# Optimization experiments

Hardware: AMD Instinct MI355X
Metric: run time of the kernel (lower is better)

## Reference

```python
import jax, jax.numpy as jnp
import numpy as np

T = 0.09   # softmax temperature
M = 0.7    # momentum for key-encoder update
DIM, K, B, L, P = 128, 65536, 1024, 512, 8388608

def _l2norm(x, axis):
    return x / jnp.linalg.norm(x, axis=axis, keepdims=True)

def setup_inputs() -> dict:
    key = jax.random.key(0)
    ks = jax.random.split(key, 6)
    q = jax.random.normal(ks[0], (B, DIM), jnp.float32)
    queue = _l2norm(jax.random.normal(ks[1], (DIM, K), jnp.float32), axis=0)  # columns normalized as in __init__
    keys = jax.random.normal(ks[2], (B, DIM), jnp.float32)
    param_q = jax.random.normal(ks[3], (P,), jnp.float32)
    param_k = jax.random.normal(ks[4], (P,), jnp.float32)
    sample_idx = jax.random.randint(ks[5], (B, L), 0, K, jnp.int32)  # col 0 = positive sample index
    return {"q": q, "queue": queue, "keys": keys, "param_q": param_q,
            "param_k": param_k, "sample_idx": sample_idx, "ptr": 0}

def reference(q, queue, keys, param_q, param_k, sample_idx, ptr):
    # q = F.normalize(q, dim=1)
    qn = _l2norm(q, axis=1)
    # per-sample ragged gather of queue columns, batched: queue[:, idx] for each sample list
    cols = jnp.take(queue.T, sample_idx, axis=0)            # [B, L, DIM]
    # logits = einsum('c,ck->k', q_i, gathered_i), stacked + padded, / T
    logits = jnp.einsum('bld,bd->bl', cols, qn) / T         # [B, L]
    labels = jnp.zeros((B,), jnp.int32)                     # positive is index 0
    # momentum update of key-encoder params: k = m*k + (1-m)*q
    new_param_k = param_k * M + param_q * (1.0 - M)
    # dequeue/enqueue: queue[:, ptr:ptr+B] = normalize(keys).T (circular write)
    new_queue = jax.lax.dynamic_update_slice(queue, _l2norm(keys, axis=1).T, (0, ptr))
    return (logits, labels, new_queue, new_param_k)
```

## Files before the change

kernel.cpp:

```cpp
#include <hip/hip_runtime.h>
#include <stdint.h>

#define DIM   128
#define KCOLS 65536
#define BB    1024
#define LL    512
#define PSZ   8388608
#define INV_T (1.0f / 0.09f)
#define MOM   0.7f

#define OUT_LOGITS 0
#define OUT_LABELS (BB * LL)
#define OUT_QUEUE  (BB * LL + BB)
#define OUT_PARAMK (BB * LL + BB + DIM * KCOLS)

#define WS_QT 0

__device__ inline unsigned short f32_to_bf16(float f) {
    uint32_t u = __float_as_uint(f);
    uint32_t r = (u + 0x7fffu + ((u >> 16) & 1u)) >> 16;
    return (unsigned short)r;
}

__global__ void __launch_bounds__(256)
queue_fused_kernel(const float* __restrict__ queue,
                   const float* __restrict__ keys,
                   const int* __restrict__ ptr_p,
                   float* __restrict__ outq,
                   unsigned short* __restrict__ qt) {
    __shared__ float tile[64][DIM + 1];
    __shared__ float invn_s[64];
    int k0 = blockIdx.x * 64;
    int t  = threadIdx.x;
    int ptr   = ptr_p[0];
    int start = min(max(ptr, 0), KCOLS - BB);

    {
        int row_local = t >> 2;
        int l4        = t & 3;
        int c = k0 + row_local;
        if (c >= start && c < start + BB) {
            const float4* kr =
                (const float4*)&keys[(size_t)(c - start) * DIM + l4 * 32];
            float s = 0.f;
#pragma unroll
            for (int i = 0; i < 8; ++i) {
                float4 v = kr[i];
                s += v.x * v.x + v.y * v.y + v.z * v.z + v.w * v.w;
            }
            s += __shfl_xor(s, 1, 64);
            s += __shfl_xor(s, 2, 64);
            if (l4 == 0) invn_s[row_local] = 1.0f / sqrtf(s);
        }
    }
    __syncthreads();

    int lane16 = t & 15;
    int hi     = t >> 4;
    int kq     = lane16 * 4;
#pragma unroll
    for (int p = 0; p < 8; ++p) {
        int d = p * 16 + hi;
        float4 v = *(const float4*)&queue[(size_t)d * KCOLS + k0 + kq];
        float vv[4] = {v.x, v.y, v.z, v.w};
#pragma unroll
        for (int j = 0; j < 4; ++j) {
            tile[kq + j][d] = vv[j];
            int col = k0 + kq + j;
            if (col >= start && col < start + BB)
                vv[j] = keys[(size_t)(col - start) * DIM + d] * invn_s[kq + j];
        }
        float4 w = {vv[0], vv[1], vv[2], vv[3]};
        *(float4*)&outq[(size_t)d * KCOLS + k0 + kq] = w;
    }
    __syncthreads();
    int d0 = lane16 * 8;
#pragma unroll
    for (int ki = 0; ki < 4; ++ki) {
        int kl = hi + ki * 16;
        float f[8];
#pragma unroll
        for (int j = 0; j < 8; ++j) f[j] = tile[kl][d0 + j];
        uint4 o;
        o.x = (uint32_t)f32_to_bf16(f[0]) | ((uint32_t)f32_to_bf16(f[1]) << 16);
        o.y = (uint32_t)f32_to_bf16(f[2]) | ((uint32_t)f32_to_bf16(f[3]) << 16);
        o.z = (uint32_t)f32_to_bf16(f[4]) | ((uint32_t)f32_to_bf16(f[5]) << 16);
        o.w = (uint32_t)f32_to_bf16(f[6]) | ((uint32_t)f32_to_bf16(f[7]) << 16);
        *(uint4*)&qt[(size_t)(k0 + kl) * DIM + d0] = o;
    }
}

#define DOT8(uu, qo, dst) {                                    \
    float acc = 0.f;                                           \
    acc += qreg[(qo) + 0] * __uint_as_float((uu).x << 16);     \
    acc += qreg[(qo) + 1] * __uint_as_float((uu).x & 0xffff0000u); \
    acc += qreg[(qo) + 2] * __uint_as_float((uu).y << 16);     \
    acc += qreg[(qo) + 3] * __uint_as_float((uu).y & 0xffff0000u); \
    acc += qreg[(qo) + 4] * __uint_as_float((uu).z << 16);     \
    acc += qreg[(qo) + 5] * __uint_as_float((uu).z & 0xffff0000u); \
    acc += qreg[(qo) + 6] * __uint_as_float((uu).w << 16);     \
    acc += qreg[(qo) + 7] * __uint_as_float((uu).w & 0xffff0000u); \
    (dst) = acc; }

__global__ void __launch_bounds__(256)
logits_param_kernel(const float* __restrict__ q,
                    const unsigned short* __restrict__ qt,
                    const int* __restrict__ sidx,
                    const float* __restrict__ pq,
                    const float* __restrict__ pk,
                    float* __restrict__ out) {
    int t   = threadIdx.x;
    int bid = blockIdx.x;
    int g   = bid / 9;
    int rem = bid - g * 9;

    if (rem != 0) {
        int gid  = (g * 8 + rem - 1) * 256 + t;
        float4 a = ((const float4*)pq)[gid];
        float4 c = ((const float4*)pk)[gid];
        float4 r;
        r.x = c.x * MOM + a.x * (1.0f - MOM);
        r.y = c.y * MOM + a.y * (1.0f - MOM);
        r.z = c.z * MOM + a.z * (1.0f - MOM);
        r.w = c.w * MOM + a.w * (1.0f - MOM);
        ((float4*)(out + OUT_PARAMK))[gid] = r;
        if (gid < BB) out[OUT_LABELS + gid] = 0.0f;
        return;
    }

    int b = g;
    __shared__ int sl[LL];
#pragma unroll
    for (int l = t; l < LL; l += 256) sl[l] = sidx[b * LL + l];

    int quarter = t & 3;
    int grp     = t >> 2;

    float qreg[32];
    {
        const float* qb = q + (size_t)b * DIM;
        float s = 0.f;
#pragma unroll
        for (int j = 0; j < 4; ++j) {
            const float4* pp = (const float4*)(qb + j * 32 + quarter * 8);
            float4 v0 = pp[0], v1 = pp[1];
            qreg[j * 8 + 0] = v0.x; qreg[j * 8 + 1] = v0.y;
            qreg[j * 8 + 2] = v0.z; qreg[j * 8 + 3] = v0.w;
            qreg[j * 8 + 4] = v1.x; qreg[j * 8 + 5] = v1.y;
            qreg[j * 8 + 6] = v1.z; qreg[j * 8 + 7] = v1.w;
            s += v0.x * v0.x + v0.y * v0.y + v0.z * v0.z + v0.w * v0.w;
            s += v1.x * v1.x + v1.y * v1.y + v1.z * v1.z + v1.w * v1.w;
        }
        s += __shfl_xor(s, 1, 64);
        s += __shfl_xor(s, 2, 64);
        float inv = rsqrtf(s) * INV_T;
#pragma unroll
        for (int i = 0; i < 32; ++i) qreg[i] *= inv;
    }
    __syncthreads();

    int idxs[8];
#pragma unroll
    for (int e = 0; e < 8; ++e) idxs[e] = sl[grp + (e << 6)];

    uint4 u[4][4];
#pragma unroll
    for (int e = 0; e < 4; ++e) {
        const uint4* p = (const uint4*)(qt + (size_t)idxs[e] * DIM) + quarter;
        u[e][0] = p[0]; u[e][1] = p[4]; u[e][2] = p[8]; u[e][3] = p[12];
    }
#pragma unroll
    for (int e = 0; e < 8; ++e) {
        const int slot = e & 3;
        uint4 t0 = u[slot][0], t1 = u[slot][1], t2 = u[slot][2], t3 = u[slot][3];
        if (e < 4) {
            const uint4* p =
                (const uint4*)(qt + (size_t)idxs[e + 4] * DIM) + quarter;
            u[slot][0] = p[0]; u[slot][1] = p[4];
            u[slot][2] = p[8]; u[slot][3] = p[12];
        }
        float s0, s1, s2, s3;
        DOT8(t0,  0, s0);
        DOT8(t1,  8, s1);
        DOT8(t2, 16, s2);
        DOT8(t3, 24, s3);
        float s = (s0 + s1) + (s2 + s3);
        s += __shfl_xor(s, 1, 64);
        s += __shfl_xor(s, 2, 64);
        if (quarter == 0)
            out[OUT_LOGITS + (size_t)b * LL + grp + (e << 6)] = s;
    }
}

extern "C" void kernel_launch(void* const* d_in, const int* in_sizes, int n_in,
                              void* d_out, int out_size, void* d_ws, size_t ws_size,
                              hipStream_t stream) {
    const float* q     = (const float*)d_in[0];
    const float* queue = (const float*)d_in[1];
    const float* keys  = (const float*)d_in[2];
    const float* pq    = (const float*)d_in[3];
    const float* pk    = (const float*)d_in[4];
    const int*   sidx  = (const int*)d_in[5];
    const int*   ptr_p = (const int*)d_in[6];
    float* out = (float*)d_out;

    unsigned short* ws_qt = (unsigned short*)((char*)d_ws + WS_QT);

    queue_fused_kernel<<<KCOLS / 64, 256, 0, stream>>>(queue, keys, ptr_p,
                                                       out + OUT_QUEUE, ws_qt);
    logits_param_kernel<<<9 * BB, 256, 0, stream>>>(q, ws_qt, sidx,
                                                    pq, pk, out);
}
```

Baseline: 182.9 us.

## Partition logits gather by XCD so each XCD reads an L2-resident queue slice

Each logits block now handles 8 batch rows, but only the sample indices whose high bits match the block's XCD (g&7, which lines up with round-robin block-to-XCD placement). Indices are filtered and compacted into shared memory with LDS atomics, so each XCD gathers from a 2 MB slice of the bf16 transposed queue that can stay in its L2, instead of the whole 16 MB table. The query norm is also computed with a single wider shuffle reduction. The trade-offs are a per-row cap of 128 matches (rows over that limit would silently drop logits), uneven per-block work, and atomic compaction overhead.

New measurement: 187.3 us. 1.02x slower.

```diff
diff --git a/kernel.cpp b/kernel.cpp
--- a/kernel.cpp
+++ b/kernel.cpp
@@ -128,67 +128,109 @@
         return;
     }
 
-    int b = g;
-    __shared__ int sl[LL];
-#pragma unroll
-    for (int l = t; l < LL; l += 256) sl[l] = sidx[b * LL + l];
+    int xcd    = g & 7;
+    int b_base = (g >> 3) * 8;
+
+    __shared__ unsigned short lsl[8][128];
+    __shared__ unsigned short lsi[8][128];
+    __shared__ int cnt8[8];
+    if (t < 8) cnt8[t] = 0;
 
     int quarter = t & 3;
-    int grp     = t >> 2;
+    int qrt     = t >> 2;
+    int sub     = qrt & 7;
+    int b_local = qrt >> 3;
+    int b       = b_base + b_local;
 
     float qreg[32];
     {
+        int half = t & 31;
+        float4 v = ((const float4*)(q + (size_t)b * DIM))[half];
+        float s  = v.x * v.x + v.y * v.y + v.z * v.z + v.w * v.w;
+        s += __shfl_xor(s, 1, 64);
+        s += __shfl_xor(s, 2, 64);
+        s += __shfl_xor(s, 4, 64);
+        s += __shfl_xor(s, 8, 64);
+        s += __shfl_xor(s, 16, 64);
+        float inv = rsqrtf(s) * INV_T;
         const float* qb = q + (size_t)b * DIM;
-        float s = 0.f;
 #pragma unroll
         for (int j = 0; j < 4; ++j) {
             const float4* pp = (const float4*)(qb + j * 32 + quarter * 8);
             float4 v0 = pp[0], v1 = pp[1];
-            qreg[j * 8 + 0] = v0.x; qreg[j * 8 + 1] = v0.y;
-            qreg[j * 8 + 2] = v0.z; qreg[j * 8 + 3] = v0.w;
-            qreg[j * 8 + 4] = v1.x; qreg[j * 8 + 5] = v1.y;
-            qreg[j * 8 + 6] = v1.z; qreg[j * 8 + 7] = v1.w;
-            s += v0.x * v0.x + v0.y * v0.y + v0.z * v0.z + v0.w * v0.w;
-            s += v1.x * v1.x + v1.y * v1.y + v1.z * v1.z + v1.w * v1.w;
-        }
-        s += __shfl_xor(s, 1, 64);
-        s += __shfl_xor(s, 2, 64);
-        float inv = rsqrtf(s) * INV_T;
-#pragma unroll
-        for (int i = 0; i < 32; ++i) qreg[i] *= inv;
-    }
-    __syncthreads();
-
-    int idxs[8];
-#pragma unroll
-    for (int e = 0; e < 8; ++e) idxs[e] = sl[grp + (e << 6)];
-
-    uint4 u[4][4];
-#pragma unroll
-    for (int e = 0; e < 4; ++e) {
-        const uint4* p = (const uint4*)(qt + (size_t)idxs[e] * DIM) + quarter;
-        u[e][0] = p[0]; u[e][1] = p[4]; u[e][2] = p[8]; u[e][3] = p[12];
-    }
-#pragma unroll
-    for (int e = 0; e < 8; ++e) {
-        const int slot = e & 3;
-        uint4 t0 = u[slot][0], t1 = u[slot][1], t2 = u[slot][2], t3 = u[slot][3];
-        if (e < 4) {
-            const uint4* p =
-                (const uint4*)(qt + (size_t)idxs[e + 4] * DIM) + quarter;
-            u[slot][0] = p[0]; u[slot][1] = p[4];
-            u[slot][2] = p[8]; u[slot][3] = p[12];
-        }
-        float s0, s1, s2, s3;
-        DOT8(t0,  0, s0);
-        DOT8(t1,  8, s1);
-        DOT8(t2, 16, s2);
-        DOT8(t3, 24, s3);
-        float s = (s0 + s1) + (s2 + s3);
-        s += __shfl_xor(s, 1, 64);
-        s += __shfl_xor(s, 2, 64);
-        if (quarter == 0)
-            out[OUT_LOGITS + (size_t)b * LL + grp + (e << 6)] = s;
+            qreg[j * 8 + 0] = v0.x * inv; qreg[j * 8 + 1] = v0.y * inv;
+            qreg[j * 8 + 2] = v0.z * inv; qreg[j * 8 + 3] = v0.w * inv;
+            qreg[j * 8 + 4] = v1.x * inv; qreg[j * 8 + 5] = v1.y * inv;
+            qreg[j * 8 + 6] = v1.z * inv; qreg[j * 8 + 7] = v1.w * inv;
+        }
+    }
+    __syncthreads();
+
+    {
+        const int4* s4 = (const int4*)(sidx + (size_t)b_base * LL);
+#pragma unroll
+        for (int c = 0; c < 4; ++c) {
+            int chunk = t + c * 256;
+            int4 v  = s4[chunk];
+            int bl  = chunk >> 7;
+            int l0  = (chunk & 127) * 4;
+            int ids[4] = {v.x, v.y, v.z, v.w};
+#pragma unroll
+            for (int j = 0; j < 4; ++j) {
+                int idx = ids[j];
+                if ((idx >> 13) == xcd) {
+                    int p = atomicAdd(&cnt8[bl], 1);
+                    if (p < 128) {
+                        lsl[bl][p] = (unsigned short)(l0 + j);
+                        lsi[bl][p] = (unsigned short)(idx & 0x1FFF);
+                    }
+                }
+            }
+        }
+    }
+    __syncthreads();
+    int cb = min(cnt8[b_local], 128);
+
+    const unsigned short* qbase = qt + ((size_t)xcd << 13) * DIM;
+    float* outl = out + OUT_LOGITS + (size_t)b * LL;
+
+    for (int i = sub; i < cb; i += 16) {
+        int iB  = i + 8;
+        int lA  = lsl[b_local][i];
+        const uint4* pA =
+            (const uint4*)(qbase + (size_t)lsi[b_local][i] * DIM) + quarter;
+        uint4 a0 = pA[0], a1 = pA[4], a2 = pA[8], a3 = pA[12];
+        bool vB = iB < cb;
+        int lB = 0;
+        uint4 b0, b1, b2, b3;
+        if (vB) {
+            lB = lsl[b_local][iB];
+            const uint4* pB =
+                (const uint4*)(qbase + (size_t)lsi[b_local][iB] * DIM) + quarter;
+            b0 = pB[0]; b1 = pB[4]; b2 = pB[8]; b3 = pB[12];
+        }
+        {
+            float s0, s1, s2, s3;
+            DOT8(a0,  0, s0);
+            DOT8(a1,  8, s1);
+            DOT8(a2, 16, s2);
+            DOT8(a3, 24, s3);
+            float s = (s0 + s1) + (s2 + s3);
+            s += __shfl_xor(s, 1, 64);
+            s += __shfl_xor(s, 2, 64);
+            if (quarter == 0) outl[lA] = s;
+        }
+        if (vB) {
+            float s0, s1, s2, s3;
+            DOT8(b0,  0, s0);
+            DOT8(b1,  8, s1);
+            DOT8(b2, 16, s2);
+            DOT8(b3, 24, s3);
+            float s = (s0 + s1) + (s2 + s3);
+            s += __shfl_xor(s, 1, 64);
+            s += __shfl_xor(s, 2, 64);
+            if (quarter == 0) outl[lB] = s;
+        }
     }
 }
 
```

## Move momentum param update into queue kernel and use nontemporal streaming loads/stores

Applied to the files above, without the earlier changes.

The momentum parameter update and label zeroing move out of the logits kernel and into the queue-transpose kernel, which now interleaves queue blocks with param blocks. Streaming fp32 traffic (queue, param_q/param_k, new_queue, new_param_k) uses nontemporal loads and stores, so it does not evict the bf16 transposed queue the gather kernel reuses through cache. The logits kernel becomes a pure gather-dot kernel with one block per sample. This rebalances bandwidth-bound work between the two launches. It risks the first kernel becoming longer and serialising ahead of the gather.

New measurement: 178.3 us. 1.03x faster.

```diff
diff --git a/kernel.cpp b/kernel.cpp
--- a/kernel.cpp
+++ b/kernel.cpp
@@ -16,6 +16,8 @@
 
 #define WS_QT 0
 
+typedef float f32x4 __attribute__((ext_vector_type(4)));
+
 __device__ inline unsigned short f32_to_bf16(float f) {
     uint32_t u = __float_as_uint(f);
     uint32_t r = (u + 0x7fffu + ((u >> 16) & 1u)) >> 16;
@@ -23,15 +25,39 @@
 }
 
 __global__ void __launch_bounds__(256)
-queue_fused_kernel(const float* __restrict__ queue,
+queue_param_kernel(const float* __restrict__ queue,
                    const float* __restrict__ keys,
                    const int* __restrict__ ptr_p,
-                   float* __restrict__ outq,
+                   const float* __restrict__ pq,
+                   const float* __restrict__ pk,
+                   float* __restrict__ out,
                    unsigned short* __restrict__ qt) {
+    int bid = blockIdx.x;
+    int t   = threadIdx.x;
+
+    if (bid & 1) {
+        int c = bid >> 1;
+        const f32x4* pq4 = (const f32x4*)pq;
+        const f32x4* pk4 = (const f32x4*)pk;
+        f32x4* paramk4   = (f32x4*)(out + OUT_PARAMK);
+#pragma unroll
+        for (int i = 0; i < 8; ++i) {
+            int gid = c * 2048 + i * 256 + t;
+            f32x4 a = __builtin_nontemporal_load(pq4 + gid);
+            f32x4 b = __builtin_nontemporal_load(pk4 + gid);
+            f32x4 r = b * MOM + a * (1.0f - MOM);
+            __builtin_nontemporal_store(r, paramk4 + gid);
+        }
+        if (c == 0) {
+            f32x4 z = {0.f, 0.f, 0.f, 0.f};
+            ((f32x4*)(out + OUT_LABELS))[t] = z;
+        }
+        return;
+    }
+
     __shared__ float tile[64][DIM + 1];
     __shared__ float invn_s[64];
-    int k0 = blockIdx.x * 64;
-    int t  = threadIdx.x;
+    int k0 = (bid >> 1) * 64;
     int ptr   = ptr_p[0];
     int start = min(max(ptr, 0), KCOLS - BB);
 
@@ -61,7 +87,8 @@
 #pragma unroll
     for (int p = 0; p < 8; ++p) {
         int d = p * 16 + hi;
-        float4 v = *(const float4*)&queue[(size_t)d * KCOLS + k0 + kq];
+        f32x4 v = __builtin_nontemporal_load(
+            (const f32x4*)&queue[(size_t)d * KCOLS + k0 + kq]);
         float vv[4] = {v.x, v.y, v.z, v.w};
 #pragma unroll
         for (int j = 0; j < 4; ++j) {
@@ -70,8 +97,9 @@
             if (col >= start && col < start + BB)
                 vv[j] = keys[(size_t)(col - start) * DIM + d] * invn_s[kq + j];
         }
-        float4 w = {vv[0], vv[1], vv[2], vv[3]};
-        *(float4*)&outq[(size_t)d * KCOLS + k0 + kq] = w;
+        f32x4 w = {vv[0], vv[1], vv[2], vv[3]};
+        __builtin_nontemporal_store(
+            w, (f32x4*)&out[OUT_QUEUE + (size_t)d * KCOLS + k0 + kq]);
     }
     __syncthreads();
     int d0 = lane16 * 8;
@@ -103,32 +131,13 @@
     (dst) = acc; }
 
 __global__ void __launch_bounds__(256)
-logits_param_kernel(const float* __restrict__ q,
-                    const unsigned short* __restrict__ qt,
-                    const int* __restrict__ sidx,
-                    const float* __restrict__ pq,
-                    const float* __restrict__ pk,
-                    float* __restrict__ out) {
-    int t   = threadIdx.x;
-    int bid = blockIdx.x;
-    int g   = bid / 9;
-    int rem = bid - g * 9;
-
-    if (rem != 0) {
-        int gid  = (g * 8 + rem - 1) * 256 + t;
-        float4 a = ((const float4*)pq)[gid];
-        float4 c = ((const float4*)pk)[gid];
-        float4 r;
-        r.x = c.x * MOM + a.x * (1.0f - MOM);
-        r.y = c.y * MOM + a.y * (1.0f - MOM);
-        r.z = c.z * MOM + a.z * (1.0f - MOM);
-        r.w = c.w * MOM + a.w * (1.0f - MOM);
-        ((float4*)(out + OUT_PARAMK))[gid] = r;
-        if (gid < BB) out[OUT_LABELS + gid] = 0.0f;
-        return;
-    }
-
-    int b = g;
+logits_kernel(const float* __restrict__ q,
+              const unsigned short* __restrict__ qt,
+              const int* __restrict__ sidx,
+              float* __restrict__ out) {
+    int b = blockIdx.x;
+    int t = threadIdx.x;
+
     __shared__ int sl[LL];
 #pragma unroll
     for (int l = t; l < LL; l += 256) sl[l] = sidx[b * LL + l];
@@ -163,21 +172,21 @@
 #pragma unroll
     for (int e = 0; e < 8; ++e) idxs[e] = sl[grp + (e << 6)];
 
-    uint4 u[4][4];
+    uint4 w[4][4];
 #pragma unroll
     for (int e = 0; e < 4; ++e) {
         const uint4* p = (const uint4*)(qt + (size_t)idxs[e] * DIM) + quarter;
-        u[e][0] = p[0]; u[e][1] = p[4]; u[e][2] = p[8]; u[e][3] = p[12];
+        w[e][0] = p[0]; w[e][1] = p[4]; w[e][2] = p[8]; w[e][3] = p[12];
     }
 #pragma unroll
     for (int e = 0; e < 8; ++e) {
         const int slot = e & 3;
-        uint4 t0 = u[slot][0], t1 = u[slot][1], t2 = u[slot][2], t3 = u[slot][3];
+        uint4 t0 = w[slot][0], t1 = w[slot][1], t2 = w[slot][2], t3 = w[slot][3];
         if (e < 4) {
             const uint4* p =
                 (const uint4*)(qt + (size_t)idxs[e + 4] * DIM) + quarter;
-            u[slot][0] = p[0]; u[slot][1] = p[4];
-            u[slot][2] = p[8]; u[slot][3] = p[12];
+            w[slot][0] = p[0]; w[slot][1] = p[4];
+            w[slot][2] = p[8]; w[slot][3] = p[12];
         }
         float s0, s1, s2, s3;
         DOT8(t0,  0, s0);
@@ -206,8 +215,7 @@
 
     unsigned short* ws_qt = (unsigned short*)((char*)d_ws + WS_QT);
 
-    queue_fused_kernel<<<KCOLS / 64, 256, 0, stream>>>(queue, keys, ptr_p,
-                                                       out + OUT_QUEUE, ws_qt);
-    logits_param_kernel<<<9 * BB, 256, 0, stream>>>(q, ws_qt, sidx,
-                                                    pq, pk, out);
-}
+    queue_param_kernel<<<2 * (KCOLS / 64), 256, 0, stream>>>(
+        queue, keys, ptr_p, pq, pk, out, ws_qt);
+    logits_kernel<<<BB, 256, 0, stream>>>(q, ws_qt, sidx, out + OUT_LOGITS);
+}
```
